# Performance work log

Hardware: AMD Instinct MI355X
Metric: run time of the kernel (lower is better)

Reference implementation:

```python
import jax, jax.numpy as jnp
import numpy as np

B, T, L, D = 4, 8, 512, 512
H, KD, VD = 8, 64, 64


def setup_inputs() -> dict:
    key = jax.random.key(0)
    ks = jax.random.split(key, 8)
    s = 0.05
    return {
        "queries": jax.random.normal(ks[0], (B, T, L, D), jnp.float32),
        "keys": jax.random.normal(ks[1], (B, T, L, D), jnp.float32),
        "values": jax.random.normal(ks[2], (B, T, L, D), jnp.float32),
        "attn_mask": jnp.ones((1, 1, 1, L, L), jnp.float32),
        "Wq": jax.random.normal(ks[3], (D, H, KD), jnp.float32) * s,
        "Wk": jax.random.normal(ks[4], (D, H, KD), jnp.float32) * s,
        "Wv": jax.random.normal(ks[5], (D, H, VD), jnp.float32) * s,
        "w_head": jax.random.normal(ks[6], (H,), jnp.float32),
        "tau": jnp.ones((1,), jnp.float32),
        "delta": jnp.zeros((1,), jnp.float32),
    }


def reference(queries, keys, values, attn_mask, Wq, Wk, Wv, w_head, tau, delta):
    # Projections: (b,t,l,d) x (d,h,e) -> (b,t,l,h,e)
    Q = jnp.einsum('btld,dhe->btlhe', queries, Wq)
    K = jnp.einsum('btld,dhe->btlhe', keys, Wk)
    V = jnp.einsum('btld,dhe->btlhe', values, Wv)
    scale = 1.0 / jnp.sqrt(jnp.asarray(KD, jnp.float32))
    # Full score tensor (b,t,h,l,s)
    scores = jnp.einsum('btlhe,btshe->bthls', Q, K)
    # de-stationary rescaling, then scale, then multiplicative mask
    scores = (scores * tau[0] + delta[0]) * scale
    scores = scores * attn_mask
    # Dropout(attn_dropout) before softmax is identity at inference
    p = jax.nn.softmax(scores, axis=-1)
    attn = jnp.einsum('bthls,btshe->bthle', p, V)
    # Per-head scalar weighted sum over heads: (b,t,h,l,e),(h)->(b,t,l,e)
    return jnp.einsum('bthle,h->btle', attn, w_head)
```

## Files before the change

kernel.cpp:

```cpp
#include <hip/hip_runtime.h>
#include <hip/hip_bf16.h>

typedef __bf16 bf16;
typedef __bf16 bf16x4 __attribute__((ext_vector_type(4)));
typedef __bf16 bf16x8 __attribute__((ext_vector_type(8)));
typedef float f32x4 __attribute__((ext_vector_type(4)));


__global__ __launch_bounds__(256) void prep_kernel(const float* __restrict__ W0,
                                                   const float* __restrict__ W1,
                                                   const float* __restrict__ W2,
                                                   bf16* __restrict__ Wt) {
    __shared__ float t[64][65];
    const float* W = (blockIdx.z == 0) ? W0 : (blockIdx.z == 1) ? W1 : W2;
    bf16* O = Wt + (size_t)blockIdx.z * 512 * 512;
    const int d0 = blockIdx.x * 64, n0 = blockIdx.y * 64;
    {
        int nl = threadIdx.x & 63, dg = threadIdx.x >> 6;
#pragma unroll
        for (int j = 0; j < 16; ++j) {
            int dl = dg + j * 4;
            t[nl][dl] = W[(size_t)(d0 + dl) * 512 + n0 + nl];
        }
    }
    __syncthreads();
    {
        int dl = threadIdx.x & 63, ng = threadIdx.x >> 6;
#pragma unroll
        for (int j = 0; j < 16; ++j) {
            int nl = ng + j * 4;
            O[(size_t)(n0 + nl) * 512 + d0 + dl] = (bf16)t[nl][dl];
        }
    }
}

__global__ __launch_bounds__(256) void proj_kernel(
    const float* __restrict__ Xq, const float* __restrict__ Xk,
    const float* __restrict__ Xv, const bf16* __restrict__ Wt,
    bf16* __restrict__ Qw, bf16* __restrict__ Kw, bf16* __restrict__ Vt) {
    __shared__ __align__(16) bf16 smem[18432];
    bf16* la = smem;
    bf16* lb = smem + 128 * 72;

    const float* X = (blockIdx.z == 0) ? Xq : (blockIdx.z == 1) ? Xk : Xv;
    const bf16* W  = Wt + (size_t)blockIdx.z * 512 * 512;
    bf16* Out      = (blockIdx.z == 0) ? Qw : (blockIdx.z == 1) ? Kw : Vt;

    const int tid = threadIdx.x, wave = tid >> 6, lane = tid & 63;
    const int quad = lane >> 4, lc = lane & 15;
    const int wm = wave & 1, wn = wave >> 1;
    const int m0 = blockIdx.x * 128, n0 = blockIdx.y * 128;

    f32x4 acc[4][4];
#pragma unroll
    for (int ms = 0; ms < 4; ++ms)
#pragma unroll
        for (int ns = 0; ns < 4; ++ns) acc[ms][ns] = (f32x4){0.f, 0.f, 0.f, 0.f};

    const int ar = tid >> 4, ac = tid & 15;
    const int br = tid >> 3, bc = tid & 7;

    float4 xr[8];
    bf16x8 wr[4];
#pragma unroll
    for (int i = 0; i < 8; ++i)
        xr[i] = *(const float4*)&X[(size_t)(m0 + ar + i * 16) * 512 + ac * 4];
#pragma unroll
    for (int i = 0; i < 4; ++i)
        wr[i] = *(const bf16x8*)&W[(size_t)(n0 + br + i * 32) * 512 + bc * 8];

    for (int kb = 0; kb < 512; kb += 64) {
        __syncthreads();
#pragma unroll
        for (int i = 0; i < 8; ++i) {
            float4 x = xr[i];
            bf16x4 p;
            p[0] = (bf16)x.x; p[1] = (bf16)x.y; p[2] = (bf16)x.z; p[3] = (bf16)x.w;
            *(bf16x4*)&la[(ar + i * 16) * 72 + ac * 4] = p;
        }
#pragma unroll
        for (int i = 0; i < 4; ++i)
            *(bf16x8*)&lb[(br + i * 32) * 72 + bc * 8] = wr[i];
        __syncthreads();
        if (kb < 448) {
            int kn = kb + 64;
#pragma unroll
            for (int i = 0; i < 8; ++i)
                xr[i] = *(const float4*)&X[(size_t)(m0 + ar + i * 16) * 512 + kn + ac * 4];
#pragma unroll
            for (int i = 0; i < 4; ++i)
                wr[i] = *(const bf16x8*)&W[(size_t)(n0 + br + i * 32) * 512 + kn + bc * 8];
        }
#pragma unroll
        for (int kk = 0; kk < 2; ++kk) {
            bf16x8 af[4], bfr[4];
#pragma unroll
            for (int ms = 0; ms < 4; ++ms)
                af[ms] = *(bf16x8*)&la[(wm * 64 + ms * 16 + lc) * 72 + kk * 32 + quad * 8];
#pragma unroll
            for (int ns = 0; ns < 4; ++ns)
                bfr[ns] = *(bf16x8*)&lb[(wn * 64 + ns * 16 + lc) * 72 + kk * 32 + quad * 8];
#pragma unroll
            for (int ms = 0; ms < 4; ++ms)
#pragma unroll
                for (int ns = 0; ns < 4; ++ns)
                    acc[ms][ns] = __builtin_amdgcn_mfma_f32_16x16x32_bf16(
                        af[ms], bfr[ns], acc[ms][ns], 0, 0, 0);
        }
    }
    __syncthreads();
    bf16* lds_c = smem;
    if (blockIdx.z != 2) {
#pragma unroll
        for (int ms = 0; ms < 4; ++ms)
#pragma unroll
            for (int ns = 0; ns < 4; ++ns)
#pragma unroll
                for (int r = 0; r < 4; ++r)
                    lds_c[(wm * 64 + ms * 16 + quad * 4 + r) * 136 +
                          wn * 64 + ns * 16 + lc] = (bf16)acc[ms][ns][r];
    } else {
#pragma unroll
        for (int ms = 0; ms < 4; ++ms)
#pragma unroll
            for (int ns = 0; ns < 4; ++ns)
#pragma unroll
                for (int r = 0; r < 4; ++r)
                    lds_c[(wn * 64 + ns * 16 + lc) * 136 +
                          wm * 64 + ms * 16 + quad * 4 + r] = (bf16)acc[ms][ns][r];
    }
    __syncthreads();
    const int bt = m0 >> 9, l0 = m0 & 511;
    if (blockIdx.z != 2) {
        const int ec = tid & 7, rg = tid >> 3;
#pragma unroll
        for (int hc = 0; hc < 2; ++hc) {
            int h = (n0 >> 6) + hc;
#pragma unroll
            for (int p = 0; p < 4; ++p) {
                int row = rg + p * 32;
                bf16x8 v = *(bf16x8*)&lds_c[row * 136 + hc * 64 + ec * 8];
                *(bf16x8*)&Out[(((size_t)bt * 8 + h) * 512 + l0 + row) * 64 + ec * 8] = v;
            }
        }
    } else {
        const int rowp = lane >> 2, cc = lane & 3;
#pragma unroll
        for (int pr = 0; pr < 2; ++pr) {
            int row = wave * 32 + pr * 16 + rowp;
            int h = (n0 >> 6) + (row >> 6);
            int e = row & 63;
            bf16* dst = Out + (((size_t)bt * 8 + h) * 64 + e) * 512 + l0;
#pragma unroll
            for (int pc = 0; pc < 4; ++pc) {
                int mc = cc + pc * 4;
                *(bf16x8*)&dst[mc * 8] = *(bf16x8*)&lds_c[row * 136 + mc * 8];
            }
        }
    }
}

__global__ __launch_bounds__(256, 4) void attn_kernel(
    const bf16* __restrict__ Qw, const bf16* __restrict__ Kw,
    const bf16* __restrict__ Vt, const float* __restrict__ mask,
    const float* __restrict__ w_head, const float* __restrict__ tau,
    const float* __restrict__ delta, float* __restrict__ out) {
    __shared__ __align__(16) bf16 lds_k[64 * 72];
    __shared__ __align__(16) bf16 lds_vt[64 * 72];
    __shared__ __align__(16) bf16 lds_p[4][2][16 * 64];

    const int tid  = threadIdx.x;
    const int wave = tid >> 6;
    const int lane = tid & 63;
    const int quad = lane >> 4;
    const int lc   = lane & 15;
    const int b    = blockIdx.x;
    const int bth  = b & 255;
    const int qquad = b >> 8;
    const int bt   = bth >> 3;
    const int h    = bth & 7;

    const bf16* Qh  = Qw + (size_t)bth * (512 * 64);
    const bf16* Kh  = Kw + (size_t)bth * (512 * 64);
    const bf16* VtH = Vt + (size_t)bth * (512 * 64);

    const float tauf   = tau[0];
    const float deltaf = delta[0];
    const float scale  = 0.125f;
    const float wh     = w_head[h];

    const int q0 = qquad * 128 + wave * 32;
    const int swz = 2 * (lc & 7);

    bf16x8 qfA[2], qfB[2];
#pragma unroll
    for (int kk = 0; kk < 2; ++kk) {
        qfA[kk] = *(const bf16x8*)&Qh[(size_t)(q0 + lc) * 64 + kk * 32 + quad * 8];
        qfB[kk] = *(const bf16x8*)&Qh[(size_t)(q0 + 16 + lc) * 64 + kk * 32 + quad * 8];
    }

    f32x4 oA[4], oB[4];
#pragma unroll
    for (int ns = 0; ns < 4; ++ns) {
        oA[ns] = (f32x4){0.f, 0.f, 0.f, 0.f};
        oB[ns] = (f32x4){0.f, 0.f, 0.f, 0.f};
    }
    float lA = 0.f, lB = 0.f;

    const int srow = tid >> 3, scc = tid & 7;
    bf16x8 kr[2], vr[2];
#pragma unroll
    for (int j = 0; j < 2; ++j) {
        int row = srow + j * 32;
        kr[j] = *(const bf16x8*)&Kh[(size_t)row * 64 + scc * 8];
        vr[j] = *(const bf16x8*)&VtH[(size_t)row * 512 + scc * 8];
    }

    const size_t mrowA = (size_t)(q0 + lc) * 512;
    const size_t mrowB = (size_t)(q0 + 16 + lc) * 512;

    for (int c = 0; c < 8; ++c) {
        const int s0 = c * 64;
        __syncthreads();
#pragma unroll
        for (int j = 0; j < 2; ++j) {
            int row = srow + j * 32;
            *(bf16x8*)&lds_k[row * 72 + scc * 8] = kr[j];
            *(bf16x8*)&lds_vt[row * 72 + scc * 8] = vr[j];
        }
        __syncthreads();
        if (c < 7) {
            int s0n = s0 + 64;
#pragma unroll
            for (int j = 0; j < 2; ++j) {
                int row = srow + j * 32;
                kr[j] = *(const bf16x8*)&Kh[(size_t)(s0n + row) * 64 + scc * 8];
                vr[j] = *(const bf16x8*)&VtH[(size_t)row * 512 + s0n + scc * 8];
            }
        }
        f32x4 stA[4], stB[4];
#pragma unroll
        for (int ns = 0; ns < 4; ++ns) {
            stA[ns] = (f32x4){0.f, 0.f, 0.f, 0.f};
            stB[ns] = (f32x4){0.f, 0.f, 0.f, 0.f};
        }
#pragma unroll
        for (int kk = 0; kk < 2; ++kk)
#pragma unroll
            for (int ns = 0; ns < 4; ++ns) {
                bf16x8 ka = *(bf16x8*)&lds_k[(ns * 16 + lc) * 72 + kk * 32 + quad * 8];
                stA[ns] = __builtin_amdgcn_mfma_f32_16x16x32_bf16(ka, qfA[kk], stA[ns], 0, 0, 0);
                stB[ns] = __builtin_amdgcn_mfma_f32_16x16x32_bf16(ka, qfB[kk], stB[ns], 0, 0, 0);
            }
#pragma unroll
        for (int ns = 0; ns < 4; ++ns) {
            f32x4 mA = *(const f32x4*)&mask[mrowA + s0 + ns * 16 + quad * 4];
            f32x4 mB = *(const f32x4*)&mask[mrowB + s0 + ns * 16 + quad * 4];
            bf16x4 pbA, pbB;
#pragma unroll
            for (int r = 0; r < 4; ++r) {
                float pA = __expf((stA[ns][r] * tauf + deltaf) * scale * mA[r]);
                float pB = __expf((stB[ns][r] * tauf + deltaf) * scale * mB[r]);
                lA += pA; lB += pB;
                pbA[r] = (bf16)pA; pbB[r] = (bf16)pB;
            }
            int up = (ns * 4 + quad) ^ swz;
            *(bf16x4*)&lds_p[wave][0][lc * 64 + up * 4] = pbA;
            *(bf16x4*)&lds_p[wave][1][lc * 64 + up * 4] = pbB;
        }
#pragma unroll
        for (int kk = 0; kk < 2; ++kk) {
            int u0 = (8 * kk + 2 * quad) ^ swz;
            bf16x8 aaA = *(bf16x8*)&lds_p[wave][0][lc * 64 + u0 * 4];
            bf16x8 aaB = *(bf16x8*)&lds_p[wave][1][lc * 64 + u0 * 4];
#pragma unroll
            for (int ns = 0; ns < 4; ++ns) {
                bf16x8 bb = *(bf16x8*)&lds_vt[(ns * 16 + lc) * 72 + kk * 32 + quad * 8];
                oA[ns] = __builtin_amdgcn_mfma_f32_16x16x32_bf16(aaA, bb, oA[ns], 0, 0, 0);
                oB[ns] = __builtin_amdgcn_mfma_f32_16x16x32_bf16(aaB, bb, oB[ns], 0, 0, 0);
            }
        }
    }
    lA += __shfl_xor(lA, 16, 64);
    lA += __shfl_xor(lA, 32, 64);
    lB += __shfl_xor(lB, 16, 64);
    lB += __shfl_xor(lB, 32, 64);
#pragma unroll
    for (int r = 0; r < 4; ++r) {
        float lrA = __shfl(lA, quad * 4 + r, 64);
        float lrB = __shfl(lB, quad * 4 + r, 64);
        float ivA = wh / lrA, ivB = wh / lrB;
        int qqA = q0 + quad * 4 + r;
        int qqB = q0 + 16 + quad * 4 + r;
#pragma unroll
        for (int ns = 0; ns < 4; ++ns) {
            int e = ns * 16 + lc;
            atomicAdd(&out[((size_t)bt * 512 + qqA) * 64 + e], oA[ns][r] * ivA);
            atomicAdd(&out[((size_t)bt * 512 + qqB) * 64 + e], oB[ns][r] * ivB);
        }
    }
}

extern "C" void kernel_launch(void* const* d_in, const int* in_sizes, int n_in,
                              void* d_out, int out_size, void* d_ws, size_t ws_size,
                              hipStream_t stream) {
    const float* queries = (const float*)d_in[0];
    const float* keys    = (const float*)d_in[1];
    const float* values  = (const float*)d_in[2];
    const float* mask    = (const float*)d_in[3];
    const float* Wq      = (const float*)d_in[4];
    const float* Wk      = (const float*)d_in[5];
    const float* Wv      = (const float*)d_in[6];
    const float* w_head  = (const float*)d_in[7];
    const float* tau     = (const float*)d_in[8];
    const float* delta   = (const float*)d_in[9];

    char* ws = (char*)d_ws;
    bf16* Qw = (bf16*)(ws);
    bf16* Kw = (bf16*)(ws + 16777216ull);
    bf16* Vt = (bf16*)(ws + 33554432ull);
    bf16* Wt = (bf16*)(ws + 50331648ull);

    hipMemsetAsync(d_out, 0, (size_t)out_size * sizeof(float), stream);

    prep_kernel<<<dim3(8, 8, 3), 256, 0, stream>>>(Wq, Wk, Wv, Wt);

    proj_kernel<<<dim3(128, 4, 3), 256, 0, stream>>>(queries, keys, values, Wt,
                                                     Qw, Kw, Vt);

    attn_kernel<<<1024, 256, 0, stream>>>(Qw, Kw, Vt, mask, w_head, tau, delta,
                                          (float*)d_out);
}
```

Before: 230.2 us.

## Double-buffer K/V tiles, keep P in registers, prepack mask to bf16

The attention kernel now double-buffers K and V^T in LDS, which removes one barrier per chunk and lets the global loads for chunk c+2 overlap compute. The P tile stays in registers and feeds 16x16x16 MFMAs directly instead of going through an LDS round trip. The mask is prepacked into a bf16 layout matched to the MFMA fragments, which halves mask traffic, and scaling is folded into exp2. Proj_kernel block indices are also remapped, probably for cache locality. Costs are the extra prep work, more LDS, and the smaller MFMA shape issuing more instructions.

```diff
diff --git a/kernel.cpp b/kernel.cpp
--- a/kernel.cpp
+++ b/kernel.cpp
@@ -7,10 +7,48 @@
 typedef float f32x4 __attribute__((ext_vector_type(4)));
 
 
+#if __has_builtin(__builtin_amdgcn_exp2f)
+#define EXP2(x) __builtin_amdgcn_exp2f(x)
+#else
+#define EXP2(x) exp2f(x)
+#endif
+
+static __device__ __forceinline__ f32x4 mfma16(bf16x4 a, bf16x4 b, f32x4 c) {
+#if __has_builtin(__builtin_amdgcn_mfma_f32_16x16x16bf16_1k)
+    return __builtin_amdgcn_mfma_f32_16x16x16bf16_1k(a, b, c, 0, 0, 0);
+#else
+    asm("v_mfma_f32_16x16x16_bf16 %0, %1, %2, %0" : "+v"(c) : "v"(a), "v"(b));
+    return c;
+#endif
+}
+
 __global__ __launch_bounds__(256) void prep_kernel(const float* __restrict__ W0,
                                                    const float* __restrict__ W1,
                                                    const float* __restrict__ W2,
-                                                   bf16* __restrict__ Wt) {
+                                                   const float* __restrict__ maskf,
+                                                   bf16* __restrict__ Wt,
+                                                   bf16* __restrict__ Mp) {
+    if (blockIdx.z == 3) {
+        const int bid = blockIdx.y * 8 + blockIdx.x;
+        const int t0 = bid * 256 + threadIdx.x;
+        const float4* m4 = (const float4*)maskf;
+#pragma unroll
+        for (int j = 0; j < 4; ++j) {
+            int idx = t0 + j * 16384;
+            int q = idx >> 7;
+            int sc = idx & 127;
+            int cc = sc >> 4;
+            int ns = (sc >> 2) & 3;
+            int qd = sc & 3;
+            float4 v = m4[idx];
+            bf16x4 o;
+            o[0] = (bf16)v.x; o[1] = (bf16)v.y; o[2] = (bf16)v.z; o[3] = (bf16)v.w;
+            size_t off = ((((size_t)(q >> 4) * 8 + cc) * 4 + ns) * 4 + qd) * 64 +
+                         (q & 15) * 4;
+            *(bf16x4*)&Mp[off] = o;
+        }
+        return;
+    }
     __shared__ float t[64][65];
     const float* W = (blockIdx.z == 0) ? W0 : (blockIdx.z == 1) ? W1 : W2;
     bf16* O = Wt + (size_t)blockIdx.z * 512 * 512;
@@ -49,7 +87,11 @@
     const int tid = threadIdx.x, wave = tid >> 6, lane = tid & 63;
     const int quad = lane >> 4, lc = lane & 15;
     const int wm = wave & 1, wn = wave >> 1;
-    const int m0 = blockIdx.x * 128, n0 = blockIdx.y * 128;
+    const int bid = blockIdx.x + (blockIdx.y << 7);
+    const int jj = bid >> 3;
+    const int yy = jj & 3;
+    const int xt = (bid & 7) * 16 + (jj >> 2);
+    const int m0 = xt * 128, n0 = yy * 128;
 
     f32x4 acc[4][4];
 #pragma unroll
@@ -162,12 +204,11 @@
 
 __global__ __launch_bounds__(256, 4) void attn_kernel(
     const bf16* __restrict__ Qw, const bf16* __restrict__ Kw,
-    const bf16* __restrict__ Vt, const float* __restrict__ mask,
+    const bf16* __restrict__ Vt, const bf16* __restrict__ Mp,
     const float* __restrict__ w_head, const float* __restrict__ tau,
     const float* __restrict__ delta, float* __restrict__ out) {
-    __shared__ __align__(16) bf16 lds_k[64 * 72];
-    __shared__ __align__(16) bf16 lds_vt[64 * 72];
-    __shared__ __align__(16) bf16 lds_p[4][2][16 * 64];
+    __shared__ __align__(16) bf16 lds_k[2][64 * 72];
+    __shared__ __align__(16) bf16 lds_vt[2][64 * 72];
 
     const int tid  = threadIdx.x;
     const int wave = tid >> 6;
@@ -184,13 +225,14 @@
     const bf16* Kh  = Kw + (size_t)bth * (512 * 64);
     const bf16* VtH = Vt + (size_t)bth * (512 * 64);
 
-    const float tauf   = tau[0];
-    const float deltaf = delta[0];
-    const float scale  = 0.125f;
-    const float wh     = w_head[h];
+    const float L2E = 1.4426950408889634f;
+    const float ts = tau[0] * 0.125f * L2E;
+    const float ds = delta[0] * 0.125f * L2E;
+    const float wh = w_head[h];
 
     const int q0 = qquad * 128 + wave * 32;
-    const int swz = 2 * (lc & 7);
+    const size_t mbA = (size_t)(q0 >> 4) * 8192 + lane * 4;
+    const size_t mbB = mbA + 8192;
 
     bf16x8 qfA[2], qfB[2];
 #pragma unroll
@@ -209,33 +251,30 @@
 
     const int srow = tid >> 3, scc = tid & 7;
     bf16x8 kr[2], vr[2];
-#pragma unroll
-    for (int j = 0; j < 2; ++j) {
-        int row = srow + j * 32;
-        kr[j] = *(const bf16x8*)&Kh[(size_t)row * 64 + scc * 8];
-        vr[j] = *(const bf16x8*)&VtH[(size_t)row * 512 + scc * 8];
-    }
-
-    const size_t mrowA = (size_t)(q0 + lc) * 512;
-    const size_t mrowB = (size_t)(q0 + 16 + lc) * 512;
+    kr[0] = *(const bf16x8*)&Kh[(size_t)srow * 64 + scc * 8];
+    kr[1] = *(const bf16x8*)&Kh[(size_t)(srow + 32) * 64 + scc * 8];
+    vr[0] = *(const bf16x8*)&VtH[(size_t)srow * 512 + scc * 8];
+    vr[1] = *(const bf16x8*)&VtH[(size_t)(srow + 32) * 512 + scc * 8];
+    *(bf16x8*)&lds_k[0][srow * 72 + scc * 8] = kr[0];
+    *(bf16x8*)&lds_k[0][(srow + 32) * 72 + scc * 8] = kr[1];
+    *(bf16x8*)&lds_vt[0][srow * 72 + scc * 8] = vr[0];
+    *(bf16x8*)&lds_vt[0][(srow + 32) * 72 + scc * 8] = vr[1];
+    kr[0] = *(const bf16x8*)&Kh[(size_t)(64 + srow) * 64 + scc * 8];
+    kr[1] = *(const bf16x8*)&Kh[(size_t)(64 + srow + 32) * 64 + scc * 8];
+    vr[0] = *(const bf16x8*)&VtH[(size_t)srow * 512 + 64 + scc * 8];
+    vr[1] = *(const bf16x8*)&VtH[(size_t)(srow + 32) * 512 + 64 + scc * 8];
 
     for (int c = 0; c < 8; ++c) {
-        const int s0 = c * 64;
+        const int buf = c & 1;
         __syncthreads();
-#pragma unroll
-        for (int j = 0; j < 2; ++j) {
-            int row = srow + j * 32;
-            *(bf16x8*)&lds_k[row * 72 + scc * 8] = kr[j];
-            *(bf16x8*)&lds_vt[row * 72 + scc * 8] = vr[j];
-        }
-        __syncthreads();
-        if (c < 7) {
-            int s0n = s0 + 64;
-#pragma unroll
-            for (int j = 0; j < 2; ++j) {
-                int row = srow + j * 32;
-                kr[j] = *(const bf16x8*)&Kh[(size_t)(s0n + row) * 64 + scc * 8];
-                vr[j] = *(const bf16x8*)&VtH[(size_t)row * 512 + s0n + scc * 8];
+        bf16x4 mA[4], mB[4];
+        {
+            const size_t mc = mbA + (size_t)c * 1024;
+            const size_t md = mbB + (size_t)c * 1024;
+#pragma unroll
+            for (int ns = 0; ns < 4; ++ns) {
+                mA[ns] = *(const bf16x4*)&Mp[mc + ns * 256];
+                mB[ns] = *(const bf16x4*)&Mp[md + ns * 256];
             }
         }
         f32x4 stA[4], stB[4];
@@ -248,38 +287,46 @@
         for (int kk = 0; kk < 2; ++kk)
 #pragma unroll
             for (int ns = 0; ns < 4; ++ns) {
-                bf16x8 ka = *(bf16x8*)&lds_k[(ns * 16 + lc) * 72 + kk * 32 + quad * 8];
+                bf16x8 ka = *(bf16x8*)&lds_k[buf][(ns * 16 + lc) * 72 + kk * 32 + quad * 8];
                 stA[ns] = __builtin_amdgcn_mfma_f32_16x16x32_bf16(ka, qfA[kk], stA[ns], 0, 0, 0);
                 stB[ns] = __builtin_amdgcn_mfma_f32_16x16x32_bf16(ka, qfB[kk], stB[ns], 0, 0, 0);
             }
+        if (c < 7) {
+            const int nb = buf ^ 1;
+            *(bf16x8*)&lds_k[nb][srow * 72 + scc * 8] = kr[0];
+            *(bf16x8*)&lds_k[nb][(srow + 32) * 72 + scc * 8] = kr[1];
+            *(bf16x8*)&lds_vt[nb][srow * 72 + scc * 8] = vr[0];
+            *(bf16x8*)&lds_vt[nb][(srow + 32) * 72 + scc * 8] = vr[1];
+            if (c < 6) {
+                const int s0n = (c + 2) * 64;
+                kr[0] = *(const bf16x8*)&Kh[(size_t)(s0n + srow) * 64 + scc * 8];
+                kr[1] = *(const bf16x8*)&Kh[(size_t)(s0n + srow + 32) * 64 + scc * 8];
+                vr[0] = *(const bf16x8*)&VtH[(size_t)srow * 512 + s0n + scc * 8];
+                vr[1] = *(const bf16x8*)&VtH[(size_t)(srow + 32) * 512 + s0n + scc * 8];
+            }
+        }
+        bf16x4 paA[4], paB[4];
 #pragma unroll
         for (int ns = 0; ns < 4; ++ns) {
-            f32x4 mA = *(const f32x4*)&mask[mrowA + s0 + ns * 16 + quad * 4];
-            f32x4 mB = *(const f32x4*)&mask[mrowB + s0 + ns * 16 + quad * 4];
-            bf16x4 pbA, pbB;
 #pragma unroll
             for (int r = 0; r < 4; ++r) {
-                float pA = __expf((stA[ns][r] * tauf + deltaf) * scale * mA[r]);
-                float pB = __expf((stB[ns][r] * tauf + deltaf) * scale * mB[r]);
+                float eA = (stA[ns][r] * ts + ds) * (float)mA[ns][r];
+                float eB = (stB[ns][r] * ts + ds) * (float)mB[ns][r];
+                float pA = EXP2(eA);
+                float pB = EXP2(eB);
                 lA += pA; lB += pB;
-                pbA[r] = (bf16)pA; pbB[r] = (bf16)pB;
-            }
-            int up = (ns * 4 + quad) ^ swz;
-            *(bf16x4*)&lds_p[wave][0][lc * 64 + up * 4] = pbA;
-            *(bf16x4*)&lds_p[wave][1][lc * 64 + up * 4] = pbB;
-        }
-#pragma unroll
-        for (int kk = 0; kk < 2; ++kk) {
-            int u0 = (8 * kk + 2 * quad) ^ swz;
-            bf16x8 aaA = *(bf16x8*)&lds_p[wave][0][lc * 64 + u0 * 4];
-            bf16x8 aaB = *(bf16x8*)&lds_p[wave][1][lc * 64 + u0 * 4];
+                paA[ns][r] = (bf16)pA;
+                paB[ns][r] = (bf16)pB;
+            }
+        }
+#pragma unroll
+        for (int ks = 0; ks < 4; ++ks)
 #pragma unroll
             for (int ns = 0; ns < 4; ++ns) {
-                bf16x8 bb = *(bf16x8*)&lds_vt[(ns * 16 + lc) * 72 + kk * 32 + quad * 8];
-                oA[ns] = __builtin_amdgcn_mfma_f32_16x16x32_bf16(aaA, bb, oA[ns], 0, 0, 0);
-                oB[ns] = __builtin_amdgcn_mfma_f32_16x16x32_bf16(aaB, bb, oB[ns], 0, 0, 0);
-            }
-        }
+                bf16x4 vv = *(bf16x4*)&lds_vt[buf][(ns * 16 + lc) * 72 + ks * 16 + quad * 4];
+                oA[ns] = mfma16(paA[ks], vv, oA[ns]);
+                oB[ns] = mfma16(paB[ks], vv, oB[ns]);
+            }
     }
     lA += __shfl_xor(lA, 16, 64);
     lA += __shfl_xor(lA, 32, 64);
@@ -320,14 +367,15 @@
     bf16* Kw = (bf16*)(ws + 16777216ull);
     bf16* Vt = (bf16*)(ws + 33554432ull);
     bf16* Wt = (bf16*)(ws + 50331648ull);
+    bf16* Mp = (bf16*)(ws + 51904512ull);
 
     hipMemsetAsync(d_out, 0, (size_t)out_size * sizeof(float), stream);
 
-    prep_kernel<<<dim3(8, 8, 3), 256, 0, stream>>>(Wq, Wk, Wv, Wt);
+    prep_kernel<<<dim3(8, 8, 4), 256, 0, stream>>>(Wq, Wk, Wv, mask, Wt, Mp);
 
     proj_kernel<<<dim3(128, 4, 3), 256, 0, stream>>>(queries, keys, values, Wt,
                                                      Qw, Kw, Vt);
 
-    attn_kernel<<<1024, 256, 0, stream>>>(Qw, Kw, Vt, mask, w_head, tau, delta,
+    attn_kernel<<<1024, 256, 0, stream>>>(Qw, Kw, Vt, Mp, w_head, tau, delta,
                                           (float*)d_out);
 }
```

After: 229.8 us. No clear change (-0.2%).
